# Performance work log

Measured on AMD Instinct MI355X. Metric: run time of the kernel, lower is better.

Reference implementation:

```python
import jax, jax.numpy as jnp
import numpy as np

DN = ('NCHW', 'OIHW', 'NCHW')

def conv2d(x, w, b, stride=1, pad=1):
    y = jax.lax.conv_general_dilated(x, w, (stride, stride), ((pad, pad), (pad, pad)),
                                     dimension_numbers=DN)
    return y + b[None, :, None, None]

def deconv2d(x, w, b):
    # PyTorch ConvTranspose2d(k=3, s=2, p=1, output_padding=1): weight is (I, O, kh, kw);
    # equivalent to conv with lhs_dilation=2, pad (k-1-p, k-1-p+output_padding)=(1,2), flipped kernel.
    wt = jnp.flip(w, (2, 3)).transpose(1, 0, 2, 3)  # -> (O, I, kh, kw)
    y = jax.lax.conv_general_dilated(x, wt, (1, 1), ((1, 2), (1, 2)),
                                     lhs_dilation=(2, 2), dimension_numbers=DN)
    return y + b[None, :, None, None]

def gru_cell(x, h, wg, bg, wc, bc):
    # standard ConvGRU: gates from cat(x, h), candidate from cat(x, r*h)
    g = jax.nn.sigmoid(conv2d(jnp.concatenate([x, h], axis=1), wg, bg, 1, 1))
    r, u = jnp.split(g, 2, axis=1)
    c = jnp.tanh(conv2d(jnp.concatenate([x, r * h], axis=1), wc, bc, 1, 1))
    return u * h + (1.0 - u) * c

def setup_inputs() -> dict:
    key = jax.random.key(0)
    ks = jax.random.split(key, 20)
    C_IN, BC = 32, 8  # in_channels, base_channels
    B, D, H, W = 1, 48, 256, 320
    s = 0.05
    def w(k, shape):
        return jax.random.normal(k, shape, jnp.float32) * s
    return {
        'volume_variance': jax.random.normal(ks[0], (B, C_IN, D, H, W), jnp.float32),
        'conv1_w': w(ks[1], (BC, C_IN, 3, 3)),       'conv1_b': jnp.zeros((BC,), jnp.float32),
        'gru1_wg': w(ks[2], (2 * BC, 2 * BC, 3, 3)), 'gru1_bg': jnp.zeros((2 * BC,), jnp.float32),
        'gru1_wc': w(ks[3], (BC, 2 * BC, 3, 3)),     'gru1_bc': jnp.zeros((BC,), jnp.float32),
        'conv2_w': w(ks[4], (2 * BC, BC, 3, 3)),     'conv2_b': jnp.zeros((2 * BC,), jnp.float32),
        'gru2_wg': w(ks[5], (4 * BC, 4 * BC, 3, 3)), 'gru2_bg': jnp.zeros((4 * BC,), jnp.float32),
        'gru2_wc': w(ks[6], (2 * BC, 4 * BC, 3, 3)), 'gru2_bc': jnp.zeros((2 * BC,), jnp.float32),
        'up1_w': w(ks[7], (2 * BC, BC, 3, 3)),       'up1_b': jnp.zeros((BC,), jnp.float32),   # ConvTranspose (I,O,kh,kw)
        'up2_w': w(ks[8], (BC, 1, 3, 3)),            'up2_b': jnp.zeros((1,), jnp.float32),
    }

def reference(volume_variance, conv1_w, conv1_b, gru1_wg, gru1_bg, gru1_wc, gru1_bc,
              conv2_w, conv2_b, gru2_wg, gru2_bg, gru2_wc, gru2_bc,
              up1_w, up1_b, up2_w, up2_b):
    B, F, D, H, W = volume_variance.shape
    dt = volume_variance.dtype
    xs = jnp.moveaxis(volume_variance, 2, 0)  # (D, B, F, H, W)
    s1 = jnp.zeros((B, 8, H, W), dt)
    s2 = jnp.zeros((B, 16, H // 2, W // 2), dt)

    def step(carry, cost):
        s1, s2 = carry
        c1 = jax.nn.relu(conv2d(cost, conv1_w, conv1_b, 1, 1))
        s1 = gru_cell(c1, s1, gru1_wg, gru1_bg, gru1_wc, gru1_bc)
        c2 = jax.nn.relu(conv2d(s1, conv2_w, conv2_b, 2, 1))
        s2 = gru_cell(c2, s2, gru2_wg, gru2_bg, gru2_wc, gru2_bc)
        up1 = deconv2d(s2, up1_w, up1_b)          # back to (B, 8, H, W)
        u = jax.nn.relu(up1 + s1)
        out = deconv2d(u, up2_w, up2_b)           # (B, 1, 2H, 2W)
        return (s1, s2), out

    _, outs = jax.lax.scan(step, (s1, s2), xs)    # outs: (D, B, 1, 2H, 2W)
    return jnp.moveaxis(outs[:, :, 0], 0, 1)      # (B, D, 2H, 2W)
```

## Files before the change

### kernel.cpp

```cpp
#include <hip/hip_runtime.h>

#define DD 48
#define HF 256
#define WF 320
#define HH 128
#define WH 160
#define NPF (HF * WF)
#define NPH (HH * WH)
#define S1SZ (8 * NPF)
#define S2SZ (16 * NPH)

__device__ __forceinline__ float sigf(float x) { return 1.0f / (1.0f + __expf(-x)); }
__device__ __forceinline__ float tanh_(float x) {
    float e = __expf(2.0f * x);
    return 1.0f - 2.0f / (e + 1.0f);
}


template<int Ht, int Wt>
__device__ __forceinline__ void taps2v(int y0, int x, int* off, float* msk) {
    const int xm = max(x - 1, 0), xp = min(x + 1, Wt - 1);
    const float cm0 = (x > 0) ? 1.0f : 0.0f;
    const float cm2 = (x < Wt - 1) ? 1.0f : 0.0f;
#pragma unroll
    for (int r = 0; r < 4; ++r) {
        const int yy = y0 - 1 + r;
        const float rm = ((unsigned)yy < (unsigned)Ht) ? 1.0f : 0.0f;
        const int rb = min(max(yy, 0), Ht - 1) * Wt;
        off[r * 3 + 0] = rb + xm; msk[r * 3 + 0] = rm * cm0;
        off[r * 3 + 1] = rb + x;  msk[r * 3 + 1] = rm;
        off[r * 3 + 2] = rb + xp; msk[r * 3 + 2] = rm * cm2;
    }
}

template<int CI, int COUT>
__device__ __forceinline__ void acc2v(
    const float* __restrict__ in, int cs,
    const float* __restrict__ w, int wcs,
    const int* off, const float* msk,
    float* a0, float* a1)
{
#pragma unroll 2
    for (int ci = 0; ci < CI; ++ci) {
        const float* p = in + ci * cs;
        float v[12];
#pragma unroll
        for (int k = 0; k < 12; ++k) v[k] = p[off[k]] * msk[k];
        const float* wp = w + ci * 9;
#pragma unroll
        for (int j = 0; j < COUT; ++j) {
            const float* wc = wp + j * wcs;
#pragma unroll
            for (int r = 0; r < 3; ++r) {
#pragma unroll
                for (int c = 0; c < 3; ++c) {
                    a0[j] = fmaf(v[r * 3 + c],       wc[r * 3 + c], a0[j]);
                    a1[j] = fmaf(v[(r + 1) * 3 + c], wc[r * 3 + c], a1[j]);
                }
            }
        }
    }
}

__device__ __forceinline__ void conv1_role(
    const float* __restrict__ x, const float* __restrict__ w,
    const float* __restrict__ b, float* __restrict__ o_slice,
    int dsl, int pb)
{
    const int t = pb * 256 + threadIdx.x;
    const int xc = t % WF;
    const int yb = (t / WF) * 4;
    const float* __restrict__ xin = x + (long)dsl * NPF;
    const int cxm = max(xc - 1, 0), cxp = min(xc + 1, WF - 1);
    const float cmm = (xc > 0) ? 1.0f : 0.0f;
    const float cmp = (xc < WF - 1) ? 1.0f : 0.0f;
    int off[18]; float msk[18];
#pragma unroll
    for (int r = 0; r < 6; ++r) {
        const int yy = yb - 1 + r;
        const float rm = ((unsigned)yy < (unsigned)HF) ? 1.0f : 0.0f;
        const int rb = min(max(yy, 0), HF - 1) * WF;
        off[r * 3 + 0] = rb + cxm; msk[r * 3 + 0] = rm * cmm;
        off[r * 3 + 1] = rb + xc;  msk[r * 3 + 1] = rm;
        off[r * 3 + 2] = rb + cxp; msk[r * 3 + 2] = rm * cmp;
    }
    float acc[4][8];
#pragma unroll
    for (int j = 0; j < 8; ++j) {
        const float bj = b[j];
#pragma unroll
        for (int q = 0; q < 4; ++q) acc[q][j] = bj;
    }
#pragma unroll 2
    for (int ci = 0; ci < 32; ++ci) {
        const float* p = xin + (long)ci * (DD * NPF);
        float v[18];
#pragma unroll
        for (int k = 0; k < 18; ++k) v[k] = p[off[k]] * msk[k];
        const float* wp = w + ci * 9;
#pragma unroll
        for (int j = 0; j < 8; ++j) {
            const float* wc = wp + j * (32 * 9);
#pragma unroll
            for (int q = 0; q < 4; ++q) {
#pragma unroll
                for (int r = 0; r < 3; ++r) {
                    acc[q][j] = fmaf(v[(q + r) * 3 + 0], wc[r * 3 + 0], acc[q][j]);
                    acc[q][j] = fmaf(v[(q + r) * 3 + 1], wc[r * 3 + 1], acc[q][j]);
                    acc[q][j] = fmaf(v[(q + r) * 3 + 2], wc[r * 3 + 2], acc[q][j]);
                }
            }
        }
    }
    float* o = o_slice + yb * WF + xc;
#pragma unroll
    for (int j = 0; j < 8; ++j)
#pragma unroll
        for (int q = 0; q < 4; ++q)
            o[j * NPF + q * WF] = fmaxf(acc[q][j], 0.0f);
}

__device__ __forceinline__ void conv1p_role(
    const float* __restrict__ x, const float* __restrict__ w,
    const float* __restrict__ b, float* __restrict__ o_slice,
    int dsl, int pb)
{
    const int t = pb * 256 + threadIdx.x;
    const int y = t / WF, xc = t - y * WF;
    const float* __restrict__ xin = x + (long)dsl * NPF;
    const int cxm = max(xc - 1, 0), cxp = min(xc + 1, WF - 1);
    const float cmm = (xc > 0) ? 1.0f : 0.0f;
    const float cmp = (xc < WF - 1) ? 1.0f : 0.0f;
    int off[9]; float msk[9];
#pragma unroll
    for (int r = 0; r < 3; ++r) {
        const int yy = y - 1 + r;
        const float rm = ((unsigned)yy < (unsigned)HF) ? 1.0f : 0.0f;
        const int rb = min(max(yy, 0), HF - 1) * WF;
        off[r * 3 + 0] = rb + cxm; msk[r * 3 + 0] = rm * cmm;
        off[r * 3 + 1] = rb + xc;  msk[r * 3 + 1] = rm;
        off[r * 3 + 2] = rb + cxp; msk[r * 3 + 2] = rm * cmp;
    }
    float acc[8];
#pragma unroll
    for (int j = 0; j < 8; ++j) acc[j] = b[j];
#pragma unroll 2
    for (int ci = 0; ci < 32; ++ci) {
        const float* p = xin + (long)ci * (DD * NPF);
        float v[9];
#pragma unroll
        for (int k = 0; k < 9; ++k) v[k] = p[off[k]] * msk[k];
        const float* wp = w + ci * 9;
#pragma unroll
        for (int j = 0; j < 8; ++j) {
            const float* wc = wp + j * (32 * 9);
#pragma unroll
            for (int k = 0; k < 9; ++k) acc[j] = fmaf(v[k], wc[k], acc[j]);
        }
    }
    float* o = o_slice + t;
#pragma unroll
    for (int j = 0; j < 8; ++j) o[j * NPF] = fmaxf(acc[j], 0.0f);
}

__global__ __launch_bounds__(256) void k_conv1(
    const float* __restrict__ x, const float* __restrict__ w,
    const float* __restrict__ b, float* __restrict__ out,
    int d0, int ostride)
{
    conv1_role(x, w, b, out + (long)blockIdx.z * ostride, d0 + blockIdx.z, blockIdx.x);
}

template<int C, int Ht, int Wt, int CO>
__device__ __forceinline__ void gates_role(
    const float* __restrict__ a, const float* __restrict__ s,
    const float* __restrict__ w, const float* __restrict__ b,
    float* __restrict__ rh, float* __restrict__ u, int pb, int cog)
{
    constexpr int NP = Ht * Wt;
    const int t = pb * 256 + threadIdx.x;
    const int x = t % Wt, y0 = (t / Wt) * 2;
    const int co0 = cog * CO;
    int off[12]; float msk[12];
    taps2v<Ht, Wt>(y0, x, off, msk);
    float a0[CO], a1[CO];
#pragma unroll
    for (int j = 0; j < CO; ++j) { a0[j] = b[co0 + j]; a1[j] = b[co0 + j]; }
    acc2v<C, CO>(a, NP, w + co0 * (2 * C * 9), 2 * C * 9, off, msk, a0, a1);
    acc2v<C, CO>(s, NP, w + co0 * (2 * C * 9) + C * 9, 2 * C * 9, off, msk, a0, a1);
    const int p0 = y0 * Wt + x;
    if (co0 < C) {
#pragma unroll
        for (int j = 0; j < CO; ++j) {
            int o = (co0 + j) * NP + p0;
            rh[o]      = sigf(a0[j]) * s[o];
            rh[o + Wt] = sigf(a1[j]) * s[o + Wt];
        }
    } else {
#pragma unroll
        for (int j = 0; j < CO; ++j) {
            int o = (co0 - C + j) * NP + p0;
            u[o]      = sigf(a0[j]);
            u[o + Wt] = sigf(a1[j]);
        }
    }
}

template<int C, int Ht, int Wt, int CO>
__device__ __forceinline__ void cand_role(
    const float* __restrict__ a, const float* __restrict__ rh,
    const float* __restrict__ w, const float* __restrict__ b,
    const float* __restrict__ u, const float* __restrict__ sprev,
    float* __restrict__ sout, int pb, int cog)
{
    constexpr int NP = Ht * Wt;
    const int t = pb * 256 + threadIdx.x;
    const int x = t % Wt, y0 = (t / Wt) * 2;
    const int co0 = cog * CO;
    int off[12]; float msk[12];
    taps2v<Ht, Wt>(y0, x, off, msk);
    float a0[CO], a1[CO];
#pragma unroll
    for (int j = 0; j < CO; ++j) { a0[j] = b[co0 + j]; a1[j] = b[co0 + j]; }
    acc2v<C, CO>(a, NP, w + co0 * (2 * C * 9), 2 * C * 9, off, msk, a0, a1);
    acc2v<C, CO>(rh, NP, w + co0 * (2 * C * 9) + C * 9, 2 * C * 9, off, msk, a0, a1);
    const int p0 = y0 * Wt + x;
#pragma unroll
    for (int j = 0; j < CO; ++j) {
        int o = (co0 + j) * NP + p0;
        float c0 = tanh_(a0[j]);
        float c1 = tanh_(a1[j]);
        sout[o]      = fmaf(u[o],      sprev[o]      - c0, c0);
        sout[o + Wt] = fmaf(u[o + Wt], sprev[o + Wt] - c1, c1);
    }
}

__device__ __forceinline__ void conv2_role(
    const float* __restrict__ s1, const float* __restrict__ w,
    const float* __restrict__ b, float* __restrict__ c2, int pb, int cog)
{
    const int t = pb * 256 + threadIdx.x;
    const int x = t % WH, yp = t / WH;
    const int y0 = 2 * yp;
    const int co0 = cog * 8;
    int off[15]; float msk[15];
    {
        const int cxm = max(2 * x - 1, 0);
        const float cmm = (x > 0) ? 1.0f : 0.0f;
#pragma unroll
        for (int r = 0; r < 5; ++r) {
            const int yy = 4 * yp - 1 + r;
            const float rm = (yy >= 0) ? 1.0f : 0.0f;
            const int rb = max(yy, 0) * WF;
            off[r * 3 + 0] = rb + cxm;       msk[r * 3 + 0] = rm * cmm;
            off[r * 3 + 1] = rb + 2 * x;     msk[r * 3 + 1] = rm;
            off[r * 3 + 2] = rb + 2 * x + 1; msk[r * 3 + 2] = rm;
        }
    }
    float a0[8], a1[8];
#pragma unroll
    for (int j = 0; j < 8; ++j) { a0[j] = b[co0 + j]; a1[j] = b[co0 + j]; }
#pragma unroll 2
    for (int ci = 0; ci < 8; ++ci) {
        const float* p = s1 + ci * NPF;
        float v[15];
#pragma unroll
        for (int k = 0; k < 15; ++k) v[k] = p[off[k]] * msk[k];
        const float* wp = w + co0 * 72 + ci * 9;
#pragma unroll
        for (int j = 0; j < 8; ++j) {
            const float* wc = wp + j * 72;
#pragma unroll
            for (int r = 0; r < 3; ++r) {
#pragma unroll
                for (int c = 0; c < 3; ++c) {
                    a0[j] = fmaf(v[r * 3 + c],       wc[r * 3 + c], a0[j]);
                    a1[j] = fmaf(v[(r + 2) * 3 + c], wc[r * 3 + c], a1[j]);
                }
            }
        }
    }
    const int p0 = y0 * WH + x;
#pragma unroll
    for (int j = 0; j < 8; ++j) {
        c2[(co0 + j) * NPH + p0]      = fmaxf(a0[j], 0.0f);
        c2[(co0 + j) * NPH + p0 + WH] = fmaxf(a1[j], 0.0f);
    }
}

__device__ __forceinline__ void up1_role(
    const float* __restrict__ s2, const float* __restrict__ w,
    const float* __restrict__ b, const float* __restrict__ s1,
    float* __restrict__ ubuf, int pb)
{
    const int q = pb * 256 + threadIdx.x;
    const int r = q / WH, c = q - r * WH;
    const int dc = (c + 1 < WH) ? 1 : 0;
    const int dr = (r + 1 < HH) ? WH : 0;
    const float mc = (c + 1 < WH) ? 1.0f : 0.0f;
    const float mr = (r + 1 < HH) ? 1.0f : 0.0f;
    const float mrc = mc * mr;
    float a00[8], a01[8], a10[8], a11[8];
#pragma unroll
    for (int j = 0; j < 8; ++j) { a00[j] = b[j]; a01[j] = b[j]; a10[j] = b[j]; a11[j] = b[j]; }
#pragma unroll 2
    for (int ci = 0; ci < 16; ++ci) {
        const float* p = s2 + ci * NPH + r * WH + c;
        float v00 = p[0];
        float v01 = p[dc] * mc;
        float v10 = p[dr] * mr;
        float v11 = p[dr + dc] * mrc;
        const float* wp = w + ci * 8 * 9;
#pragma unroll
        for (int j = 0; j < 8; ++j) {
            const float* wc = wp + j * 9;
            a00[j] = fmaf(v00, wc[4], a00[j]);
            a01[j] = fmaf(v01, wc[3], fmaf(v00, wc[5], a01[j]));
            a10[j] = fmaf(v10, wc[1], fmaf(v00, wc[7], a10[j]));
            a11[j] = fmaf(v11, wc[0], fmaf(v10, wc[2], fmaf(v01, wc[6], fmaf(v00, wc[8], a11[j]))));
        }
    }
    const int o0 = (2 * r) * WF + 2 * c;
#pragma unroll
    for (int j = 0; j < 8; ++j) {
        int o = j * NPF + o0;
        ubuf[o]          = fmaxf(a00[j] + s1[o], 0.0f);
        ubuf[o + 1]      = fmaxf(a01[j] + s1[o + 1], 0.0f);
        ubuf[o + WF]     = fmaxf(a10[j] + s1[o + WF], 0.0f);
        ubuf[o + WF + 1] = fmaxf(a11[j] + s1[o + WF + 1], 0.0f);
    }
}

__device__ __forceinline__ void up2_role(
    const float* __restrict__ u, const float* __restrict__ w,
    const float* __restrict__ b, float* __restrict__ oslice, int pb)
{
    const int q = pb * 256 + threadIdx.x;
    const int r = q / WF, c = q - r * WF;
    const int dc = (c + 1 < WF) ? 1 : 0;
    const int dr = (r + 1 < HF) ? WF : 0;
    const float mc = (c + 1 < WF) ? 1.0f : 0.0f;
    const float mr = (r + 1 < HF) ? 1.0f : 0.0f;
    const float mrc = mc * mr;
    const float b0 = b[0];
    float a00 = b0, a01 = b0, a10 = b0, a11 = b0;
#pragma unroll 2
    for (int ci = 0; ci < 8; ++ci) {
        const float* p = u + ci * NPF + r * WF + c;
        float v00 = p[0];
        float v01 = p[dc] * mc;
        float v10 = p[dr] * mr;
        float v11 = p[dr + dc] * mrc;
        const float* wc = w + ci * 9;
        a00 = fmaf(v00, wc[4], a00);
        a01 = fmaf(v01, wc[3], fmaf(v00, wc[5], a01));
        a10 = fmaf(v10, wc[1], fmaf(v00, wc[7], a10));
        a11 = fmaf(v11, wc[0], fmaf(v10, wc[2], fmaf(v01, wc[6], fmaf(v00, wc[8], a11))));
    }
    float* o = oslice + (2 * r) * 640 + 2 * c;
    o[0] = a00; o[1] = a01; o[640] = a10; o[641] = a11;
}

__global__ __launch_bounds__(256) void k_stepA(
    const float* __restrict__ x, const float* __restrict__ w1,
    const float* __restrict__ b1, float* __restrict__ c1_all,
    const float* __restrict__ s1_all,
    const float* __restrict__ wg1, const float* __restrict__ bg1,
    float* __restrict__ rh1, float* __restrict__ ug1,
    const float* __restrict__ c2_all, const float* __restrict__ s2_all,
    const float* __restrict__ wg2, const float* __restrict__ bg2,
    float* __restrict__ rh2, float* __restrict__ ug2,
    const float* __restrict__ wu1, const float* __restrict__ bu1,
    float* __restrict__ ubuf,
    int d1, int d2, int dcv1, int du1)
{
    const int bid = blockIdx.x;
    if (bid < 320) {
        if (d1 < 0) return;
        gates_role<8, HF, WF, 8>(c1_all + (long)d1 * S1SZ, s1_all + (long)d1 * S1SZ,
                                 wg1, bg1, rh1, ug1, bid % 160, bid / 160);
    } else if (bid < 640) {
        if (d2 < 0) return;
        const int bb = bid - 320;
        gates_role<16, HH, WH, 4>(c2_all + (long)d2 * S2SZ, s2_all + (long)d2 * S2SZ,
                                  wg2, bg2, rh2, ug2, bb % 40, bb / 40);
    } else if (bid < 960) {
        if (dcv1 < 0) return;
        conv1p_role(x, w1, b1, c1_all + (long)dcv1 * S1SZ, dcv1, bid - 640);
    } else {
        if (du1 < 0) return;
        up1_role(s2_all + (long)(du1 + 1) * S2SZ, wu1, bu1,
                 s1_all + (long)(du1 + 1) * S1SZ, ubuf, bid - 960);
    }
}

__global__ __launch_bounds__(256) void k_stepB(
    const float* __restrict__ c1_all, float* __restrict__ s1_all,
    const float* __restrict__ wc1, const float* __restrict__ bc1,
    const float* __restrict__ rh1, const float* __restrict__ ug1,
    const float* __restrict__ w2, const float* __restrict__ b2,
    float* __restrict__ c2_all, float* __restrict__ s2_all,
    const float* __restrict__ wc2, const float* __restrict__ bc2,
    const float* __restrict__ rh2, const float* __restrict__ ug2,
    const float* __restrict__ wu2, const float* __restrict__ bu2,
    const float* __restrict__ ubuf, float* __restrict__ out,
    int d1, int dc, int d2, int du2)
{
    const int bid = blockIdx.x;
    if (bid < 160) {
        if (d1 < 0) return;
        cand_role<8, HF, WF, 8>(c1_all + (long)d1 * S1SZ, rh1, wc1, bc1, ug1,
                                s1_all + (long)d1 * S1SZ, s1_all + (long)(d1 + 1) * S1SZ,
                                bid, 0);
    } else if (bid < 240) {
        if (dc < 0) return;
        const int bb = bid - 160;
        conv2_role(s1_all + (long)(dc + 1) * S1SZ, w2, b2,
                   c2_all + (long)dc * S2SZ, bb % 40, bb / 40);
    } else if (bid < 400) {
        if (d2 < 0) return;
        const int bb = bid - 240;
        cand_role<16, HH, WH, 4>(c2_all + (long)d2 * S2SZ, rh2, wc2, bc2, ug2,
                                 s2_all + (long)d2 * S2SZ, s2_all + (long)(d2 + 1) * S2SZ,
                                 bb % 40, bb / 40);
    } else {
        if (du2 < 0) return;
        up2_role(ubuf, wu2, bu2, out + (long)du2 * (512 * 640), bid - 400);
    }
}

template<int C, int Ht, int Wt, int CO>
__global__ __launch_bounds__(256) void k_gates(
    const float* __restrict__ a, const float* __restrict__ s,
    const float* __restrict__ w, const float* __restrict__ b,
    float* __restrict__ rh, float* __restrict__ u)
{ gates_role<C, Ht, Wt, CO>(a, s, w, b, rh, u, blockIdx.x, blockIdx.y); }

template<int C, int Ht, int Wt, int CO>
__global__ __launch_bounds__(256) void k_cand(
    const float* __restrict__ a, const float* __restrict__ rh,
    const float* __restrict__ w, const float* __restrict__ b,
    const float* __restrict__ u, const float* __restrict__ sprev,
    float* __restrict__ sout)
{ cand_role<C, Ht, Wt, CO>(a, rh, w, b, u, sprev, sout, blockIdx.x, blockIdx.y); }

__global__ __launch_bounds__(256) void k_conv2w(
    const float* __restrict__ s1, const float* __restrict__ w,
    const float* __restrict__ b, float* __restrict__ c2)
{ conv2_role(s1, w, b, c2, blockIdx.x, blockIdx.y); }

__global__ __launch_bounds__(256) void k_up1(
    const float* __restrict__ s2b, int zs2,
    const float* __restrict__ w, const float* __restrict__ b,
    const float* __restrict__ s1b, int zs1,
    float* __restrict__ ub, int zu)
{
    up1_role(s2b + (long)blockIdx.z * zs2, w, b,
             s1b + (long)blockIdx.z * zs1, ub + (long)blockIdx.z * zu, blockIdx.x);
}

__global__ __launch_bounds__(256) void k_up2(
    const float* __restrict__ ub, int zu,
    const float* __restrict__ w, const float* __restrict__ b,
    float* __restrict__ out, int d0)
{
    up2_role(ub + (long)blockIdx.z * zu, w, b,
             out + (long)(d0 + blockIdx.z) * (512 * 640), blockIdx.x);
}

extern "C" void kernel_launch(void* const* d_in, const int* in_sizes, int n_in,
                              void* d_out, int out_size, void* d_ws, size_t ws_size,
                              hipStream_t stream)
{
    const float* x   = (const float*)d_in[0];
    const float* w1  = (const float*)d_in[1];
    const float* b1  = (const float*)d_in[2];
    const float* wg1 = (const float*)d_in[3];
    const float* bg1 = (const float*)d_in[4];
    const float* wc1 = (const float*)d_in[5];
    const float* bc1 = (const float*)d_in[6];
    const float* w2  = (const float*)d_in[7];
    const float* b2  = (const float*)d_in[8];
    const float* wg2 = (const float*)d_in[9];
    const float* bg2 = (const float*)d_in[10];
    const float* wc2 = (const float*)d_in[11];
    const float* bc2 = (const float*)d_in[12];
    const float* wu1 = (const float*)d_in[13];
    const float* bu1 = (const float*)d_in[14];
    const float* wu2 = (const float*)d_in[15];
    const float* bu2 = (const float*)d_in[16];
    float* out = (float*)d_out;
    float* ws = (float*)d_ws;

    {
        float* p = ws;
        float* s1_all = p; p += 49L * S1SZ;
        float* s2_all = p; p += 49L * S2SZ;
        float* c2_all = p; p += 48L * S2SZ;
        float* rh1 = p; p += S1SZ;
        float* ug1 = p; p += S1SZ;
        float* rh2 = p; p += S2SZ;
        float* ug2 = p; p += S2SZ;
        float* ubuf = p; p += S1SZ;
        float* c1_all = p; p += 48L * S1SZ;
        const size_t need = (size_t)(p - ws) * sizeof(float);
        if (ws_size >= need) {
            hipMemsetAsync(s1_all, 0, (size_t)S1SZ * sizeof(float), stream);
            hipMemsetAsync(s2_all, 0, (size_t)S2SZ * sizeof(float), stream);

            k_conv1<<<dim3(80, 1, 2), 256, 0, stream>>>(x, w1, b1, c1_all, 0, S1SZ);
            for (int d = 0; d <= 50; ++d) {
                const int g1  = (d < 48) ? d : -1;
                const int g2  = (d >= 2 && d <= 49) ? d - 2 : -1;
                const int cv1 = (d + 2 < 48) ? d + 2 : -1;
                const int u1  = (d >= 3) ? d - 3 : -1;
                const int cv  = (d >= 1 && d <= 48) ? d - 1 : -1;
                k_stepA<<<dim3(1040), 256, 0, stream>>>(
                    x, w1, b1, c1_all, s1_all, wg1, bg1, rh1, ug1,
                    c2_all, s2_all, wg2, bg2, rh2, ug2,
                    wu1, bu1, ubuf, g1, g2, cv1, u1);
                k_stepB<<<dim3(720), 256, 0, stream>>>(
                    c1_all, s1_all, wc1, bc1, rh1, ug1,
                    w2, b2, c2_all, s2_all, wc2, bc2, rh2, ug2,
                    wu2, bu2, ubuf, out, g1, cv, g2, u1);
            }
            return;
        }
    }

    {
        float* p = ws;
        float* s1 = p; p += S1SZ;
        float* s2 = p; p += S2SZ;
        float* rh1 = p; p += S1SZ;
        float* ug1 = p; p += S1SZ;
        float* c2 = p; p += S2SZ;
        float* rh2 = p; p += S2SZ;
        float* ug2 = p; p += S2SZ;
        float* c1 = p; p += S1SZ;
        float* u = p; p += S1SZ;
        hipMemsetAsync(s1, 0, (size_t)S1SZ * sizeof(float), stream);
        hipMemsetAsync(s2, 0, (size_t)S2SZ * sizeof(float), stream);
        for (int d = 0; d < 48; ++d) {
            k_conv1<<<dim3(80, 1, 1), 256, 0, stream>>>(x, w1, b1, c1, d, 0);
            k_gates<8, HF, WF, 8><<<dim3(160, 2), 256, 0, stream>>>(c1, s1, wg1, bg1, rh1, ug1);
            k_cand <8, HF, WF, 8><<<dim3(160, 1), 256, 0, stream>>>(c1, rh1, wc1, bc1, ug1, s1, s1);
            k_conv2w<<<dim3(40, 2), 256, 0, stream>>>(s1, w2, b2, c2);
            k_gates<16, HH, WH, 8><<<dim3(40, 4), 256, 0, stream>>>(c2, s2, wg2, bg2, rh2, ug2);
            k_cand <16, HH, WH, 8><<<dim3(40, 2), 256, 0, stream>>>(c2, rh2, wc2, bc2, ug2, s2, s2);
            k_up1<<<dim3(80, 1, 1), 256, 0, stream>>>(s2, 0, wu1, bu1, s1, 0, u, 0);
            k_up2<<<dim3(320, 1, 1), 256, 0, stream>>>(u, 0, wu2, bu2, out, d);
        }
    }
}
```

Measured before the change: 3.148 ms.

## Rebalance pipelined step kernels and switch GRU convs to one-pixel-per-thread mappings

Moves the conv1 prefetch role from the first step kernel to the second, so the two per-step launches become 720 and 1040 blocks instead of 1040 and 720. The gate convolutions switch from two output rows per thread to one pixel per thread: level 1 computes all 16 gate channels per thread, and the level-2 gates and candidate use 8 channels per thread across more blocks. This aims to balance work between the two launches and raise parallelism on the half-resolution GRU. The cost is less vertical reuse of input taps and more redundant input loads per output.

```diff
diff --git a/kernel.cpp b/kernel.cpp
--- a/kernel.cpp
+++ b/kernel.cpp
@@ -16,6 +16,43 @@
     return 1.0f - 2.0f / (e + 1.0f);
 }
 
+template<int Ht, int Wt>
+__device__ __forceinline__ void taps1v(int y, int x, int* off, float* msk) {
+    const int xm = max(x - 1, 0), xp = min(x + 1, Wt - 1);
+    const float cm0 = (x > 0) ? 1.0f : 0.0f;
+    const float cm2 = (x < Wt - 1) ? 1.0f : 0.0f;
+#pragma unroll
+    for (int r = 0; r < 3; ++r) {
+        const int yy = y - 1 + r;
+        const float rm = ((unsigned)yy < (unsigned)Ht) ? 1.0f : 0.0f;
+        const int rb = min(max(yy, 0), Ht - 1) * Wt;
+        off[r * 3 + 0] = rb + xm; msk[r * 3 + 0] = rm * cm0;
+        off[r * 3 + 1] = rb + x;  msk[r * 3 + 1] = rm;
+        off[r * 3 + 2] = rb + xp; msk[r * 3 + 2] = rm * cm2;
+    }
+}
+
+template<int CI, int COUT>
+__device__ __forceinline__ void acc1(
+    const float* __restrict__ in, int cs,
+    const float* __restrict__ w, int wcs,
+    const int* off, const float* msk, float* a)
+{
+#pragma unroll 2
+    for (int ci = 0; ci < CI; ++ci) {
+        const float* p = in + ci * cs;
+        float v[9];
+#pragma unroll
+        for (int k = 0; k < 9; ++k) v[k] = p[off[k]] * msk[k];
+        const float* wp = w + ci * 9;
+#pragma unroll
+        for (int j = 0; j < COUT; ++j) {
+            const float* wc = wp + j * wcs;
+#pragma unroll
+            for (int k = 0; k < 9; ++k) a[j] = fmaf(v[k], wc[k], a[j]);
+        }
+    }
+}
 
 template<int Ht, int Wt>
 __device__ __forceinline__ void taps2v(int y0, int x, int* off, float* msk) {
@@ -128,36 +165,12 @@
     const int t = pb * 256 + threadIdx.x;
     const int y = t / WF, xc = t - y * WF;
     const float* __restrict__ xin = x + (long)dsl * NPF;
-    const int cxm = max(xc - 1, 0), cxp = min(xc + 1, WF - 1);
-    const float cmm = (xc > 0) ? 1.0f : 0.0f;
-    const float cmp = (xc < WF - 1) ? 1.0f : 0.0f;
     int off[9]; float msk[9];
-#pragma unroll
-    for (int r = 0; r < 3; ++r) {
-        const int yy = y - 1 + r;
-        const float rm = ((unsigned)yy < (unsigned)HF) ? 1.0f : 0.0f;
-        const int rb = min(max(yy, 0), HF - 1) * WF;
-        off[r * 3 + 0] = rb + cxm; msk[r * 3 + 0] = rm * cmm;
-        off[r * 3 + 1] = rb + xc;  msk[r * 3 + 1] = rm;
-        off[r * 3 + 2] = rb + cxp; msk[r * 3 + 2] = rm * cmp;
-    }
+    taps1v<HF, WF>(y, xc, off, msk);
     float acc[8];
 #pragma unroll
     for (int j = 0; j < 8; ++j) acc[j] = b[j];
-#pragma unroll 2
-    for (int ci = 0; ci < 32; ++ci) {
-        const float* p = xin + (long)ci * (DD * NPF);
-        float v[9];
-#pragma unroll
-        for (int k = 0; k < 9; ++k) v[k] = p[off[k]] * msk[k];
-        const float* wp = w + ci * 9;
-#pragma unroll
-        for (int j = 0; j < 8; ++j) {
-            const float* wc = wp + j * (32 * 9);
-#pragma unroll
-            for (int k = 0; k < 9; ++k) acc[j] = fmaf(v[k], wc[k], acc[j]);
-        }
-    }
+    acc1<32, 8>(xin, DD * NPF, w, 32 * 9, off, msk, acc);
     float* o = o_slice + t;
 #pragma unroll
     for (int j = 0; j < 8; ++j) o[j * NPF] = fmaxf(acc[j], 0.0f);
@@ -171,67 +184,107 @@
     conv1_role(x, w, b, out + (long)blockIdx.z * ostride, d0 + blockIdx.z, blockIdx.x);
 }
 
-template<int C, int Ht, int Wt, int CO>
-__device__ __forceinline__ void gates_role(
-    const float* __restrict__ a, const float* __restrict__ s,
+__device__ __forceinline__ void gates1_role(
+    const float* __restrict__ c1, const float* __restrict__ s1,
+    const float* __restrict__ w, const float* __restrict__ b,
+    float* __restrict__ rh, float* __restrict__ u, int pb)
+{
+    const int t = pb * 256 + threadIdx.x;
+    const int y = t / WF, x = t - y * WF;
+    int off[9]; float msk[9];
+    taps1v<HF, WF>(y, x, off, msk);
+    float a[16];
+#pragma unroll
+    for (int j = 0; j < 16; ++j) a[j] = b[j];
+    acc1<8, 16>(c1, NPF, w, 144, off, msk, a);
+    acc1<8, 16>(s1, NPF, w + 72, 144, off, msk, a);
+#pragma unroll
+    for (int j = 0; j < 8; ++j) {
+        const int o = j * NPF + t;
+        rh[o] = sigf(a[j]) * s1[o];
+    }
+#pragma unroll
+    for (int j = 0; j < 8; ++j)
+        u[j * NPF + t] = sigf(a[8 + j]);
+}
+
+__device__ __forceinline__ void gates2_role(
+    const float* __restrict__ c2, const float* __restrict__ s2,
     const float* __restrict__ w, const float* __restrict__ b,
     float* __restrict__ rh, float* __restrict__ u, int pb, int cog)
 {
-    constexpr int NP = Ht * Wt;
     const int t = pb * 256 + threadIdx.x;
-    const int x = t % Wt, y0 = (t / Wt) * 2;
-    const int co0 = cog * CO;
+    const int y = t / WH, x = t - y * WH;
+    const int co0 = cog * 8;
+    int off[9]; float msk[9];
+    taps1v<HH, WH>(y, x, off, msk);
+    float a[8];
+#pragma unroll
+    for (int j = 0; j < 8; ++j) a[j] = b[co0 + j];
+    const float* wb = w + co0 * 288;
+    acc1<16, 8>(c2, NPH, wb, 288, off, msk, a);
+    acc1<16, 8>(s2, NPH, wb + 144, 288, off, msk, a);
+    if (co0 < 16) {
+#pragma unroll
+        for (int j = 0; j < 8; ++j) {
+            const int o = (co0 + j) * NPH + t;
+            rh[o] = sigf(a[j]) * s2[o];
+        }
+    } else {
+#pragma unroll
+        for (int j = 0; j < 8; ++j)
+            u[(co0 - 16 + j) * NPH + t] = sigf(a[j]);
+    }
+}
+
+__device__ __forceinline__ void cand1_role(
+    const float* __restrict__ a_in, const float* __restrict__ rh,
+    const float* __restrict__ w, const float* __restrict__ b,
+    const float* __restrict__ u, const float* __restrict__ sprev,
+    float* __restrict__ sout, int pb)
+{
+    const int t = pb * 256 + threadIdx.x;
+    const int x = t % WF, y0 = (t / WF) * 2;
     int off[12]; float msk[12];
-    taps2v<Ht, Wt>(y0, x, off, msk);
-    float a0[CO], a1[CO];
-#pragma unroll
-    for (int j = 0; j < CO; ++j) { a0[j] = b[co0 + j]; a1[j] = b[co0 + j]; }
-    acc2v<C, CO>(a, NP, w + co0 * (2 * C * 9), 2 * C * 9, off, msk, a0, a1);
-    acc2v<C, CO>(s, NP, w + co0 * (2 * C * 9) + C * 9, 2 * C * 9, off, msk, a0, a1);
-    const int p0 = y0 * Wt + x;
-    if (co0 < C) {
-#pragma unroll
-        for (int j = 0; j < CO; ++j) {
-            int o = (co0 + j) * NP + p0;
-            rh[o]      = sigf(a0[j]) * s[o];
-            rh[o + Wt] = sigf(a1[j]) * s[o + Wt];
-        }
-    } else {
-#pragma unroll
-        for (int j = 0; j < CO; ++j) {
-            int o = (co0 - C + j) * NP + p0;
-            u[o]      = sigf(a0[j]);
-            u[o + Wt] = sigf(a1[j]);
-        }
-    }
-}
-
-template<int C, int Ht, int Wt, int CO>
-__device__ __forceinline__ void cand_role(
-    const float* __restrict__ a, const float* __restrict__ rh,
-    const float* __restrict__ w, const float* __restrict__ b,
-    const float* __restrict__ u, const float* __restrict__ sprev,
-    float* __restrict__ sout, int pb, int cog)
-{
-    constexpr int NP = Ht * Wt;
-    const int t = pb * 256 + threadIdx.x;
-    const int x = t % Wt, y0 = (t / Wt) * 2;
-    const int co0 = cog * CO;
-    int off[12]; float msk[12];
-    taps2v<Ht, Wt>(y0, x, off, msk);
-    float a0[CO], a1[CO];
-#pragma unroll
-    for (int j = 0; j < CO; ++j) { a0[j] = b[co0 + j]; a1[j] = b[co0 + j]; }
-    acc2v<C, CO>(a, NP, w + co0 * (2 * C * 9), 2 * C * 9, off, msk, a0, a1);
-    acc2v<C, CO>(rh, NP, w + co0 * (2 * C * 9) + C * 9, 2 * C * 9, off, msk, a0, a1);
-    const int p0 = y0 * Wt + x;
-#pragma unroll
-    for (int j = 0; j < CO; ++j) {
-        int o = (co0 + j) * NP + p0;
+    taps2v<HF, WF>(y0, x, off, msk);
+    float a0[8], a1[8];
+#pragma unroll
+    for (int j = 0; j < 8; ++j) { a0[j] = b[j]; a1[j] = b[j]; }
+    acc2v<8, 8>(a_in, NPF, w, 144, off, msk, a0, a1);
+    acc2v<8, 8>(rh, NPF, w + 72, 144, off, msk, a0, a1);
+    const int p0 = y0 * WF + x;
+#pragma unroll
+    for (int j = 0; j < 8; ++j) {
+        const int o = j * NPF + p0;
         float c0 = tanh_(a0[j]);
         float c1 = tanh_(a1[j]);
         sout[o]      = fmaf(u[o],      sprev[o]      - c0, c0);
-        sout[o + Wt] = fmaf(u[o + Wt], sprev[o + Wt] - c1, c1);
+        sout[o + WF] = fmaf(u[o + WF], sprev[o + WF] - c1, c1);
+    }
+}
+
+__device__ __forceinline__ void cand2_role(
+    const float* __restrict__ a_in, const float* __restrict__ rh,
+    const float* __restrict__ w, const float* __restrict__ b,
+    const float* __restrict__ u, const float* __restrict__ sprev,
+    float* __restrict__ sout, int pb, int cog)
+{
+    const int t = pb * 256 + threadIdx.x;
+    const int y = t / WH, x = t - y * WH;
+    const int co0 = cog * 8;
+    int off[9]; float msk[9];
+    taps1v<HH, WH>(y, x, off, msk);
+    float a[8];
+#pragma unroll
+    for (int j = 0; j < 8; ++j) a[j] = b[co0 + j];
+    const float* wb = w + co0 * 288;
+    acc1<16, 8>(a_in, NPH, wb, 288, off, msk, a);
+    acc1<16, 8>(rh, NPH, wb + 144, 288, off, msk, a);
+#pragma unroll
+    for (int j = 0; j < 8; ++j) {
+        const int o = (co0 + j) * NPH + t;
+        float c = tanh_(a[j]);
+        sout[o] = fmaf(u[o], sprev[o] - c, c);
     }
 }
 
@@ -362,9 +415,7 @@
 }
 
 __global__ __launch_bounds__(256) void k_stepA(
-    const float* __restrict__ x, const float* __restrict__ w1,
-    const float* __restrict__ b1, float* __restrict__ c1_all,
-    const float* __restrict__ s1_all,
+    const float* __restrict__ c1_all, const float* __restrict__ s1_all,
     const float* __restrict__ wg1, const float* __restrict__ bg1,
     float* __restrict__ rh1, float* __restrict__ ug1,
     const float* __restrict__ c2_all, const float* __restrict__ s2_all,
@@ -372,30 +423,29 @@
     float* __restrict__ rh2, float* __restrict__ ug2,
     const float* __restrict__ wu1, const float* __restrict__ bu1,
     float* __restrict__ ubuf,
-    int d1, int d2, int dcv1, int du1)
+    int d1, int d2, int du1)
 {
     const int bid = blockIdx.x;
     if (bid < 320) {
         if (d1 < 0) return;
-        gates_role<8, HF, WF, 8>(c1_all + (long)d1 * S1SZ, s1_all + (long)d1 * S1SZ,
-                                 wg1, bg1, rh1, ug1, bid % 160, bid / 160);
+        gates1_role(c1_all + (long)d1 * S1SZ, s1_all + (long)d1 * S1SZ,
+                    wg1, bg1, rh1, ug1, bid);
     } else if (bid < 640) {
         if (d2 < 0) return;
         const int bb = bid - 320;
-        gates_role<16, HH, WH, 4>(c2_all + (long)d2 * S2SZ, s2_all + (long)d2 * S2SZ,
-                                  wg2, bg2, rh2, ug2, bb % 40, bb / 40);
-    } else if (bid < 960) {
-        if (dcv1 < 0) return;
-        conv1p_role(x, w1, b1, c1_all + (long)dcv1 * S1SZ, dcv1, bid - 640);
+        gates2_role(c2_all + (long)d2 * S2SZ, s2_all + (long)d2 * S2SZ,
+                    wg2, bg2, rh2, ug2, bb % 80, bb / 80);
     } else {
         if (du1 < 0) return;
         up1_role(s2_all + (long)(du1 + 1) * S2SZ, wu1, bu1,
-                 s1_all + (long)(du1 + 1) * S1SZ, ubuf, bid - 960);
+                 s1_all + (long)(du1 + 1) * S1SZ, ubuf, bid - 640);
     }
 }
 
 __global__ __launch_bounds__(256) void k_stepB(
-    const float* __restrict__ c1_all, float* __restrict__ s1_all,
+    const float* __restrict__ x, const float* __restrict__ w1,
+    const float* __restrict__ b1, float* __restrict__ c1_all,
+    float* __restrict__ s1_all,
     const float* __restrict__ wc1, const float* __restrict__ bc1,
     const float* __restrict__ rh1, const float* __restrict__ ug1,
     const float* __restrict__ w2, const float* __restrict__ b2,
@@ -404,14 +454,13 @@
     const float* __restrict__ rh2, const float* __restrict__ ug2,
     const float* __restrict__ wu2, const float* __restrict__ bu2,
     const float* __restrict__ ubuf, float* __restrict__ out,
-    int d1, int dc, int d2, int du2)
+    int d1, int dc, int d2, int dcv1, int du2)
 {
     const int bid = blockIdx.x;
     if (bid < 160) {
         if (d1 < 0) return;
-        cand_role<8, HF, WF, 8>(c1_all + (long)d1 * S1SZ, rh1, wc1, bc1, ug1,
-                                s1_all + (long)d1 * S1SZ, s1_all + (long)(d1 + 1) * S1SZ,
-                                bid, 0);
+        cand1_role(c1_all + (long)d1 * S1SZ, rh1, wc1, bc1, ug1,
+                   s1_all + (long)d1 * S1SZ, s1_all + (long)(d1 + 1) * S1SZ, bid);
     } else if (bid < 240) {
         if (dc < 0) return;
         const int bb = bid - 160;
@@ -420,29 +469,43 @@
     } else if (bid < 400) {
         if (d2 < 0) return;
         const int bb = bid - 240;
-        cand_role<16, HH, WH, 4>(c2_all + (long)d2 * S2SZ, rh2, wc2, bc2, ug2,
-                                 s2_all + (long)d2 * S2SZ, s2_all + (long)(d2 + 1) * S2SZ,
-                                 bb % 40, bb / 40);
+        cand2_role(c2_all + (long)d2 * S2SZ, rh2, wc2, bc2, ug2,
+                   s2_all + (long)d2 * S2SZ, s2_all + (long)(d2 + 1) * S2SZ,
+                   bb % 80, bb / 80);
+    } else if (bid < 720) {
+        if (dcv1 < 0) return;
+        conv1p_role(x, w1, b1, c1_all + (long)dcv1 * S1SZ, dcv1, bid - 400);
     } else {
         if (du2 < 0) return;
-        up2_role(ubuf, wu2, bu2, out + (long)du2 * (512 * 640), bid - 400);
-    }
-}
-
-template<int C, int Ht, int Wt, int CO>
-__global__ __launch_bounds__(256) void k_gates(
-    const float* __restrict__ a, const float* __restrict__ s,
+        up2_role(ubuf, wu2, bu2, out + (long)du2 * (512 * 640), bid - 720);
+    }
+}
+
+__global__ __launch_bounds__(256) void k_gates1(
+    const float* __restrict__ c1, const float* __restrict__ s1,
     const float* __restrict__ w, const float* __restrict__ b,
     float* __restrict__ rh, float* __restrict__ u)
-{ gates_role<C, Ht, Wt, CO>(a, s, w, b, rh, u, blockIdx.x, blockIdx.y); }
-
-template<int C, int Ht, int Wt, int CO>
-__global__ __launch_bounds__(256) void k_cand(
+{ gates1_role(c1, s1, w, b, rh, u, blockIdx.x); }
+
+__global__ __launch_bounds__(256) void k_cand1(
     const float* __restrict__ a, const float* __restrict__ rh,
     const float* __restrict__ w, const float* __restrict__ b,
     const float* __restrict__ u, const float* __restrict__ sprev,
     float* __restrict__ sout)
-{ cand_role<C, Ht, Wt, CO>(a, rh, w, b, u, sprev, sout, blockIdx.x, blockIdx.y); }
+{ cand1_role(a, rh, w, b, u, sprev, sout, blockIdx.x); }
+
+__global__ __launch_bounds__(256) void k_gates2(
+    const float* __restrict__ c2, const float* __restrict__ s2,
+    const float* __restrict__ w, const float* __restrict__ b,
+    float* __restrict__ rh, float* __restrict__ u)
+{ gates2_role(c2, s2, w, b, rh, u, blockIdx.x % 80, blockIdx.x / 80); }
+
+__global__ __launch_bounds__(256) void k_cand2(
+    const float* __restrict__ a, const float* __restrict__ rh,
+    const float* __restrict__ w, const float* __restrict__ b,
+    const float* __restrict__ u, const float* __restrict__ sprev,
+    float* __restrict__ sout)
+{ cand2_role(a, rh, w, b, u, sprev, sout, blockIdx.x % 80, blockIdx.x / 80); }
 
 __global__ __launch_bounds__(256) void k_conv2w(
     const float* __restrict__ s1, const float* __restrict__ w,
@@ -510,19 +573,19 @@
 
             k_conv1<<<dim3(80, 1, 2), 256, 0, stream>>>(x, w1, b1, c1_all, 0, S1SZ);
             for (int d = 0; d <= 50; ++d) {
-                const int g1  = (d < 48) ? d : -1;
+                const int g1  = (d <= 47) ? d : -1;
                 const int g2  = (d >= 2 && d <= 49) ? d - 2 : -1;
-                const int cv1 = (d + 2 < 48) ? d + 2 : -1;
+                const int cv  = (d >= 1 && d <= 48) ? d - 1 : -1;
+                const int cv1 = (d <= 45) ? d + 2 : -1;
                 const int u1  = (d >= 3) ? d - 3 : -1;
-                const int cv  = (d >= 1 && d <= 48) ? d - 1 : -1;
-                k_stepA<<<dim3(1040), 256, 0, stream>>>(
-                    x, w1, b1, c1_all, s1_all, wg1, bg1, rh1, ug1,
+                k_stepA<<<dim3(720), 256, 0, stream>>>(
+                    c1_all, s1_all, wg1, bg1, rh1, ug1,
                     c2_all, s2_all, wg2, bg2, rh2, ug2,
-                    wu1, bu1, ubuf, g1, g2, cv1, u1);
-                k_stepB<<<dim3(720), 256, 0, stream>>>(
-                    c1_all, s1_all, wc1, bc1, rh1, ug1,
+                    wu1, bu1, ubuf, g1, g2, u1);
+                k_stepB<<<dim3(1040), 256, 0, stream>>>(
+                    x, w1, b1, c1_all, s1_all, wc1, bc1, rh1, ug1,
                     w2, b2, c2_all, s2_all, wc2, bc2, rh2, ug2,
-                    wu2, bu2, ubuf, out, g1, cv, g2, u1);
+                    wu2, bu2, ubuf, out, g1, cv, g2, cv1, u1);
             }
             return;
         }
@@ -543,11 +606,11 @@
         hipMemsetAsync(s2, 0, (size_t)S2SZ * sizeof(float), stream);
         for (int d = 0; d < 48; ++d) {
             k_conv1<<<dim3(80, 1, 1), 256, 0, stream>>>(x, w1, b1, c1, d, 0);
-            k_gates<8, HF, WF, 8><<<dim3(160, 2), 256, 0, stream>>>(c1, s1, wg1, bg1, rh1, ug1);
-            k_cand <8, HF, WF, 8><<<dim3(160, 1), 256, 0, stream>>>(c1, rh1, wc1, bc1, ug1, s1, s1);
+            k_gates1<<<dim3(320), 256, 0, stream>>>(c1, s1, wg1, bg1, rh1, ug1);
+            k_cand1<<<dim3(160), 256, 0, stream>>>(c1, rh1, wc1, bc1, ug1, s1, s1);
             k_conv2w<<<dim3(40, 2), 256, 0, stream>>>(s1, w2, b2, c2);
-            k_gates<16, HH, WH, 8><<<dim3(40, 4), 256, 0, stream>>>(c2, s2, wg2, bg2, rh2, ug2);
-            k_cand <16, HH, WH, 8><<<dim3(40, 2), 256, 0, stream>>>(c2, rh2, wc2, bc2, ug2, s2, s2);
+            k_gates2<<<dim3(320), 256, 0, stream>>>(c2, s2, wg2, bg2, rh2, ug2);
+            k_cand2<<<dim3(160), 256, 0, stream>>>(c2, rh2, wc2, bc2, ug2, s2, s2);
             k_up1<<<dim3(80, 1, 1), 256, 0, stream>>>(s2, 0, wu1, bu1, s1, 0, u, 0);
             k_up2<<<dim3(320, 1, 1), 256, 0, stream>>>(u, 0, wu2, bu2, out, d);
         }
```

Result: slower. 3.543 ms (+12.5%).
